# Optimization experiments

Hardware: AMD Instinct MI355X
Metric: run time of the kernel (lower is better)

The kernel has to match this reference:

```python
import jax, jax.numpy as jnp
import numpy as np

B, S, D = 4, 2048, 1024  # batch, seq_len, input_dim (= dk = dv)


def setup_inputs() -> dict:
    key = jax.random.key(0)
    kx, kq, kk, kv = jax.random.split(key, 4)
    scale = 1.0 / np.sqrt(D)
    return {
        "x": jax.random.normal(kx, (B, S, D), dtype=jnp.float32),
        "Wq": jax.random.normal(kq, (D, D), dtype=jnp.float32) * scale,
        "Wk": jax.random.normal(kk, (D, D), dtype=jnp.float32) * scale,
        "Wv": jax.random.normal(kv, (D, D), dtype=jnp.float32) * scale,
    }


def reference(x, Wq, Wk, Wv):
    # Linear projections (bias=False). W is [in, out].
    Q = jnp.einsum("bsd,de->bse", x, Wq)
    K = jnp.einsum("bsd,de->bse", x, Wk)
    V = jnp.einsum("bsd,de->bse", x, Wv)
    dk = Q.shape[-1]
    # scores: [B, S, S]
    scores = jnp.einsum("bqe,bke->bqk", Q, K) / jnp.sqrt(jnp.float32(dk))
    # causal mask: upper triangle (j > i) masked to -inf
    S_len = x.shape[1]
    causal = jnp.triu(jnp.ones((S_len, S_len), dtype=bool), k=1)
    scores = jnp.where(causal[None, :, :], -jnp.inf, scores)
    attn = jax.nn.softmax(scores, axis=-1)
    # dropout p=0.0 (eval): identity
    return jnp.einsum("bqk,bke->bqe", attn, V)
```

## Files before the change

### kernel.cpp

```cpp
#include <hip/hip_runtime.h>

#define S_LEN 2048
#define DMODEL 1024
#define NBATCH 4

typedef unsigned short u16;
typedef __bf16 bf16x8 __attribute__((ext_vector_type(8)));
typedef float f32x4 __attribute__((ext_vector_type(4)));

typedef __attribute__((address_space(3))) unsigned lds_u32;
typedef const __attribute__((address_space(1))) unsigned glb_u32;

__device__ __forceinline__ u16 f2bf(float f) {
  union { float f; unsigned u; } v;
  v.f = f;
  unsigned r = v.u + 0x7fffu + ((v.u >> 16) & 1u);
  return (u16)(r >> 16);
}

__device__ __forceinline__ float bf2f(u16 h) {
  union { unsigned u; float f; } v;
  v.u = ((unsigned)h) << 16;
  return v.f;
}

__global__ void convert_x_kernel(const float* __restrict__ x, u16* __restrict__ xb, long n) {
  long i = ((long)blockIdx.x * blockDim.x + threadIdx.x) * 4;
  long stride = (long)gridDim.x * blockDim.x * 4;
  for (; i < n; i += stride) {
    float4 v = *reinterpret_cast<const float4*>(x + i);
    ushort4 o;
    o.x = f2bf(v.x); o.y = f2bf(v.y); o.z = f2bf(v.z); o.w = f2bf(v.w);
    *reinterpret_cast<ushort4*>(xb + i) = o;
  }
}

__global__ void transpose_w_kernel(const float* __restrict__ W, u16* __restrict__ Wt) {
  __shared__ float tile[32][33];
  int tx = threadIdx.x, ty = threadIdx.y;
  int k0 = blockIdx.x * 32, n0 = blockIdx.y * 32;
#pragma unroll
  for (int i = 0; i < 32; i += 8)
    tile[ty + i][tx] = W[(long)(k0 + ty + i) * DMODEL + n0 + tx];
  __syncthreads();
#pragma unroll
  for (int i = 0; i < 32; i += 8)
    Wt[(long)(n0 + ty + i) * DMODEL + k0 + tx] = f2bf(tile[tx][ty + i]);
}


#define STG(SRCP, LD, ISB, H, T, BUFB) do { \
    const u16* _s = (SRCP) + (long)(H) * 128 * (LD) + (T) * 64; \
    char* _d = lds + (BUFB) * 65536 + ((ISB) ? 32768 : 0) + ((H) * 8 + w) * 2048; \
    __builtin_amdgcn_global_load_lds((glb_u32*)_s, (lds_u32*)_d, 16, 0, 0); \
    __builtin_amdgcn_global_load_lds((glb_u32*)(_s + 32), (lds_u32*)(_d + 1024), 16, 0, 0); \
  } while (0)

#define READ_A(QM) do { \
    _Pragma("unroll") \
    for (int _i = 0; _i < 4; ++_i) { \
      int _mp = (QM) * 8 + wm * 4 + _i; \
      af[_i][0] = *(const bf16x8*)(_Al + (_mp * 2 + 0) * 1024 + frag_off); \
      af[_i][1] = *(const bf16x8*)(_Al + (_mp * 2 + 1) * 1024 + frag_off); \
    } \
  } while (0)

#define READ_BQ(DST, QN) do { \
    _Pragma("unroll") \
    for (int _j = 0; _j < 2; ++_j) { \
      int _np = (QN) * 8 + wn * 2 + _j; \
      DST[_j][0] = *(const bf16x8*)(_Bl + (_np * 2 + 0) * 1024 + frag_off); \
      DST[_j][1] = *(const bf16x8*)(_Bl + (_np * 2 + 1) * 1024 + frag_off); \
    } \
  } while (0)

#define MFMA16(QM, QN, BREG) do { \
    _Pragma("unroll") \
    for (int _i = 0; _i < 4; ++_i) \
      _Pragma("unroll") \
      for (int _j = 0; _j < 2; ++_j) { \
        acc[QM][QN][_i][_j] = __builtin_amdgcn_mfma_f32_16x16x32_bf16(af[_i][0], BREG[_j][0], acc[QM][QN][_i][_j], 0, 0, 0); \
        acc[QM][QN][_i][_j] = __builtin_amdgcn_mfma_f32_16x16x32_bf16(af[_i][1], BREG[_j][1], acc[QM][QN][_i][_j], 0, 0, 0); \
      } \
  } while (0)

template<int CMODE, int CAUSAL>
__global__ __launch_bounds__(512, 2) void gemm256(
    const u16* __restrict__ A, const u16* __restrict__ B, void* __restrict__ Cptr,
    int lda, int ldb, int ldc, int Kdim,
    long sAz, long sBz, long sCz)
{
  int bm = blockIdx.x, bn = blockIdx.y, bz = blockIdx.z;
  if (CAUSAL == 1 && bn > bm) return;
  int Keff = Kdim;
  if (CAUSAL == 2) { int lim = (bm + 1) * 256; if (lim < Keff) Keff = lim; }
  int NT = Keff >> 6;

  const u16* Ab = A + (long)bz * sAz + (long)bm * 256 * lda;
  const u16* Bb = B + (long)bz * sBz + (long)bn * 256 * ldb;

  __shared__ char lds[131072];

  int tid = threadIdx.x;
  int lane = tid & 63, w = tid >> 6;
  int wm = w >> 2, wn = w & 3;
  int l15 = lane & 15, lhi = lane >> 4;
  int frag_off = (l15 * 64 + lhi * 16) ^ (((lane >> 3) & 1) << 5);

  int le = lane ^ ((lane >> 5) << 1);
  int lr = le >> 2;
  int kb = (le & 3) * 8;

  const u16* Asrc = Ab + (long)(w * 16 + lr) * lda + kb;
  const u16* Bsrc = Bb + (long)(w * 16 + lr) * ldb + kb;

  f32x4 acc[2][2][4][2];
#pragma unroll
  for (int a = 0; a < 2; ++a)
#pragma unroll
    for (int b = 0; b < 2; ++b)
#pragma unroll
      for (int c = 0; c < 4; ++c)
#pragma unroll
        for (int d = 0; d < 2; ++d)
          acc[a][b][c][d] = (f32x4){0.f, 0.f, 0.f, 0.f};

  STG(Asrc, lda, 0, 0, 0, 0); STG(Bsrc, ldb, 1, 0, 0, 0);
  STG(Asrc, lda, 0, 1, 0, 0); STG(Bsrc, ldb, 1, 1, 0, 0);
  STG(Asrc, lda, 0, 0, 1, 1); STG(Bsrc, ldb, 1, 0, 1, 1);
  asm volatile("s_waitcnt vmcnt(4)" ::: "memory");
  __builtin_amdgcn_s_barrier();

  for (int g = 0; g < NT; ++g) {
    int buf = g & 1;
    int t1 = g + 1; if (t1 >= NT) t1 -= NT;
    int t2 = g + 2; if (t2 >= NT) t2 -= NT;
    const char* _Al = lds + buf * 65536;
    const char* _Bl = _Al + 32768;
    bf16x8 af[4][2], b0[2][2], b1[2][2];

    READ_A(0);
    READ_BQ(b0, 0);
    STG(Asrc, lda, 0, 1, t1, buf ^ 1);
    __builtin_amdgcn_s_barrier();
    asm volatile("s_waitcnt lgkmcnt(0)" ::: "memory");
    __builtin_amdgcn_sched_barrier(0);
    __builtin_amdgcn_s_setprio(1);
    MFMA16(0, 0, b0);
    __builtin_amdgcn_s_setprio(0);
    __builtin_amdgcn_s_barrier();

    READ_BQ(b1, 1);
    STG(Bsrc, ldb, 1, 1, t1, buf ^ 1);
    __builtin_amdgcn_s_barrier();
    asm volatile("s_waitcnt lgkmcnt(0)" ::: "memory");
    __builtin_amdgcn_sched_barrier(0);
    __builtin_amdgcn_s_setprio(1);
    MFMA16(0, 1, b1);
    __builtin_amdgcn_s_setprio(0);
    __builtin_amdgcn_s_barrier();

    READ_A(1);
    STG(Asrc, lda, 0, 0, t2, buf);
    __builtin_amdgcn_s_barrier();
    asm volatile("s_waitcnt lgkmcnt(0)" ::: "memory");
    __builtin_amdgcn_sched_barrier(0);
    __builtin_amdgcn_s_setprio(1);
    MFMA16(1, 1, b1);
    __builtin_amdgcn_s_setprio(0);
    __builtin_amdgcn_s_barrier();

    STG(Bsrc, ldb, 1, 0, t2, buf);
    __builtin_amdgcn_s_barrier();
    __builtin_amdgcn_s_setprio(1);
    MFMA16(1, 0, b0);
    __builtin_amdgcn_s_setprio(0);
    asm volatile("s_waitcnt vmcnt(4)" ::: "memory");
    __builtin_amdgcn_s_barrier();
  }

  int Mbase = bm * 256, Nbase = bn * 256;
#pragma unroll
  for (int qm = 0; qm < 2; ++qm)
#pragma unroll
    for (int qn = 0; qn < 2; ++qn)
#pragma unroll
      for (int i = 0; i < 4; ++i)
#pragma unroll
        for (int j = 0; j < 2; ++j) {
          int r0 = Mbase + qm * 128 + wm * 64 + i * 16 + lhi * 4;
          int col = Nbase + qn * 128 + wn * 32 + j * 16 + l15;
          f32x4 v = acc[qm][qn][i][j];
          if constexpr (CMODE == 0) {
            float* C = (float*)Cptr + (long)bz * sCz;
#pragma unroll
            for (int r = 0; r < 4; ++r)
              C[(long)(r0 + r) * ldc + col] = v[r];
          } else if constexpr (CMODE == 1) {
            u16* C = (u16*)Cptr + (long)bz * sCz;
#pragma unroll
            for (int r = 0; r < 4; ++r)
              C[(long)(r0 + r) * ldc + col] = f2bf(v[r]);
          } else {
            if (col < 2048) {
              u16* dst = (u16*)Cptr + (col >= 1024 ? 8388608 : 0);
              int c = col & 1023;
#pragma unroll
              for (int r = 0; r < 4; ++r)
                dst[(long)(r0 + r) * 1024 + c] = f2bf(v[r]);
            } else {
              u16* Vt = (u16*)Cptr + 16777216;
              int e = col - 2048;
              int bb = r0 >> 11, s = r0 & 2047;
              ushort4 u;
              u.x = f2bf(v[0]); u.y = f2bf(v[1]); u.z = f2bf(v[2]); u.w = f2bf(v[3]);
              *reinterpret_cast<ushort4*>(Vt + ((long)bb * 1024 + e) * 2048 + s) = u;
            }
          }
        }
}

__global__ __launch_bounds__(256) void softmax1p(const u16* __restrict__ sc,
                                                 u16* __restrict__ P) {
  int q = blockIdx.x, b = blockIdx.y;
  const u16* srow = sc + ((long)b * S_LEN + q) * S_LEN;
  u16* prow = P + ((long)b * S_LEN + q) * S_LEN;
  int n = q + 1;
  int nz = ((q >> 8) + 1) << 8;
  int tid = threadIdx.x;
  int j0 = tid * 8;
  const float scale = 0.03125f;

  __shared__ float red[8];

  float vs[8];
#pragma unroll
  for (int e = 0; e < 8; ++e) vs[e] = -1e30f;
  if (j0 < n) {
    ushort4 a = *reinterpret_cast<const ushort4*>(srow + j0);
    ushort4 c = *reinterpret_cast<const ushort4*>(srow + j0 + 4);
    vs[0] = bf2f(a.x) * scale; vs[1] = bf2f(a.y) * scale;
    vs[2] = bf2f(a.z) * scale; vs[3] = bf2f(a.w) * scale;
    vs[4] = bf2f(c.x) * scale; vs[5] = bf2f(c.y) * scale;
    vs[6] = bf2f(c.z) * scale; vs[7] = bf2f(c.w) * scale;
#pragma unroll
    for (int e = 0; e < 8; ++e)
      if (j0 + e >= n) vs[e] = -1e30f;
  }

  float m = -1e30f;
#pragma unroll
  for (int e = 0; e < 8; ++e) m = fmaxf(m, vs[e]);
#pragma unroll
  for (int off = 32; off > 0; off >>= 1) m = fmaxf(m, __shfl_xor(m, off, 64));
  if ((tid & 63) == 0) red[tid >> 6] = m;
  __syncthreads();
  float ms = fmaxf(fmaxf(red[0], red[1]), fmaxf(red[2], red[3]));

  float p[8];
  float s = 0.f;
#pragma unroll
  for (int e = 0; e < 8; ++e) { p[e] = __expf(vs[e] - ms); s += (j0 + e < n) ? p[e] : 0.f; }
#pragma unroll
  for (int off = 32; off > 0; off >>= 1) s += __shfl_xor(s, off, 64);
  __syncthreads();
  if ((tid & 63) == 0) red[4 + (tid >> 6)] = s;
  __syncthreads();
  float inv = 1.f / (red[4] + red[5] + red[6] + red[7]);

  if (j0 < nz) {
    ushort4 o0, o1;
    o0.x = (j0 + 0 < n) ? f2bf(p[0] * inv) : (u16)0;
    o0.y = (j0 + 1 < n) ? f2bf(p[1] * inv) : (u16)0;
    o0.z = (j0 + 2 < n) ? f2bf(p[2] * inv) : (u16)0;
    o0.w = (j0 + 3 < n) ? f2bf(p[3] * inv) : (u16)0;
    o1.x = (j0 + 4 < n) ? f2bf(p[4] * inv) : (u16)0;
    o1.y = (j0 + 5 < n) ? f2bf(p[5] * inv) : (u16)0;
    o1.z = (j0 + 6 < n) ? f2bf(p[6] * inv) : (u16)0;
    o1.w = (j0 + 7 < n) ? f2bf(p[7] * inv) : (u16)0;
    *reinterpret_cast<ushort4*>(prow + j0) = o0;
    *reinterpret_cast<ushort4*>(prow + j0 + 4) = o1;
  }
}

extern "C" void kernel_launch(void* const* d_in, const int* in_sizes, int n_in,
                              void* d_out, int out_size, void* d_ws, size_t ws_size,
                              hipStream_t stream) {
  const float* x  = (const float*)d_in[0];
  const float* Wq = (const float*)d_in[1];
  const float* Wk = (const float*)d_in[2];
  const float* Wv = (const float*)d_in[3];
  float* out = (float*)d_out;

  char* ws = (char*)d_ws;
  u16* xb  = (u16*)(ws);
  u16* wtb = (u16*)(ws + 16777216);
  u16* Qb  = (u16*)(ws + 23068672);
  u16* Kb  = (u16*)(ws + 39845888);
  u16* Vtb = (u16*)(ws + 56623104);
  u16* scb = (u16*)(ws + 73400320);
  u16* P   = (u16*)(ws + 106954752);

  long nx = (long)NBATCH * S_LEN * DMODEL;
  convert_x_kernel<<<2048, 256, 0, stream>>>(x, xb, nx);

  dim3 tb(32, 8);
  transpose_w_kernel<<<dim3(32, 32), tb, 0, stream>>>(Wq, wtb);
  transpose_w_kernel<<<dim3(32, 32), tb, 0, stream>>>(Wk, wtb + 1024 * 1024);
  transpose_w_kernel<<<dim3(32, 32), tb, 0, stream>>>(Wv, wtb + 2 * 1024 * 1024);

  gemm256<3, 0><<<dim3(32, 12, 1), 512, 0, stream>>>(
      xb, wtb, Qb, DMODEL, DMODEL, 0, DMODEL, 0, 0, 0);

  gemm256<1, 1><<<dim3(8, 8, 4), 512, 0, stream>>>(
      Qb, Kb, scb, DMODEL, DMODEL, S_LEN, DMODEL,
      (long)S_LEN * DMODEL, (long)S_LEN * DMODEL, (long)S_LEN * S_LEN);

  softmax1p<<<dim3(S_LEN, NBATCH), 256, 0, stream>>>(scb, P);

  gemm256<0, 2><<<dim3(8, 4, 4), 512, 0, stream>>>(
      P, Vtb, out, S_LEN, S_LEN, DMODEL, S_LEN,
      (long)S_LEN * S_LEN, (long)DMODEL * S_LEN, (long)S_LEN * DMODEL);
}
```

Before: 185.7 us.

## Add XCD swizzle, 128-row BK32 GEMM, split-K causal PV, fused weight transpose

Adds an XCD-aware block remap to the GEMMs. The QKV projection and PV GEMMs move to a new 128x256 tile kernel with K-step 32 and triple buffering, so more blocks launch and load balance improves. The causal PV product is split into two K halves, with a separate add kernel summing the second-half partials into the output. The three weight-transpose launches are merged into one, and the softmax zero-fill granularity shrinks to 128 to match the new tiles. The trade-off is extra partial-sum traffic and one more launch.

```diff
diff --git a/kernel.cpp b/kernel.cpp
--- a/kernel.cpp
+++ b/kernel.cpp
@@ -23,6 +23,15 @@
   v.u = ((unsigned)h) << 16;
   return v.f;
 }
+
+#define XCD_SWZ() do { \
+    int _nwg = gridDim.x * gridDim.y * gridDim.z; \
+    int _hw = blockIdx.x + gridDim.x * (blockIdx.y + gridDim.y * blockIdx.z); \
+    int _q = _nwg >> 3; \
+    int _w = (_hw & 7) * _q + (_hw >> 3); \
+    bm = _w % gridDim.x; _w /= gridDim.x; \
+    bn = _w % gridDim.y; bz = _w / gridDim.y; \
+  } while (0)
 
 __global__ void convert_x_kernel(const float* __restrict__ x, u16* __restrict__ xb, long n) {
   long i = ((long)blockIdx.x * blockDim.x + threadIdx.x) * 4;
@@ -35,7 +44,10 @@
   }
 }
 
-__global__ void transpose_w_kernel(const float* __restrict__ W, u16* __restrict__ Wt) {
+__global__ void transpose_w3_kernel(const float* __restrict__ Wq, const float* __restrict__ Wk,
+                                    const float* __restrict__ Wv, u16* __restrict__ Wt) {
+  const float* W = blockIdx.z == 0 ? Wq : (blockIdx.z == 1 ? Wk : Wv);
+  u16* dst = Wt + (long)blockIdx.z * 1024 * 1024;
   __shared__ float tile[32][33];
   int tx = threadIdx.x, ty = threadIdx.y;
   int k0 = blockIdx.x * 32, n0 = blockIdx.y * 32;
@@ -45,9 +57,8 @@
   __syncthreads();
 #pragma unroll
   for (int i = 0; i < 32; i += 8)
-    Wt[(long)(n0 + ty + i) * DMODEL + k0 + tx] = f2bf(tile[tx][ty + i]);
-}
-
+    dst[(long)(n0 + ty + i) * DMODEL + k0 + tx] = f2bf(tile[tx][ty + i]);
+}
 
 #define STG(SRCP, LD, ISB, H, T, BUFB) do { \
     const u16* _s = (SRCP) + (long)(H) * 128 * (LD) + (T) * 64; \
@@ -84,17 +95,15 @@
       } \
   } while (0)
 
-template<int CMODE, int CAUSAL>
-__global__ __launch_bounds__(512, 2) void gemm256(
-    const u16* __restrict__ A, const u16* __restrict__ B, void* __restrict__ Cptr,
+__global__ __launch_bounds__(512, 2) void gemm256_sc(
+    const u16* __restrict__ A, const u16* __restrict__ B, u16* __restrict__ Cptr,
     int lda, int ldb, int ldc, int Kdim,
     long sAz, long sBz, long sCz)
 {
-  int bm = blockIdx.x, bn = blockIdx.y, bz = blockIdx.z;
-  if (CAUSAL == 1 && bn > bm) return;
-  int Keff = Kdim;
-  if (CAUSAL == 2) { int lim = (bm + 1) * 256; if (lim < Keff) Keff = lim; }
-  int NT = Keff >> 6;
+  int bm, bn, bz;
+  XCD_SWZ();
+  if (bn > bm) return;
+  int NT = Kdim >> 6;
 
   const u16* Ab = A + (long)bz * sAz + (long)bm * 256 * lda;
   const u16* Bb = B + (long)bz * sBz + (long)bn * 256 * ldb;
@@ -180,6 +189,7 @@
   }
 
   int Mbase = bm * 256, Nbase = bn * 256;
+  u16* C = Cptr + (long)bz * sCz;
 #pragma unroll
   for (int qm = 0; qm < 2; ++qm)
 #pragma unroll
@@ -191,33 +201,149 @@
           int r0 = Mbase + qm * 128 + wm * 64 + i * 16 + lhi * 4;
           int col = Nbase + qn * 128 + wn * 32 + j * 16 + l15;
           f32x4 v = acc[qm][qn][i][j];
-          if constexpr (CMODE == 0) {
-            float* C = (float*)Cptr + (long)bz * sCz;
-#pragma unroll
-            for (int r = 0; r < 4; ++r)
-              C[(long)(r0 + r) * ldc + col] = v[r];
-          } else if constexpr (CMODE == 1) {
-            u16* C = (u16*)Cptr + (long)bz * sCz;
-#pragma unroll
-            for (int r = 0; r < 4; ++r)
-              C[(long)(r0 + r) * ldc + col] = f2bf(v[r]);
-          } else {
-            if (col < 2048) {
-              u16* dst = (u16*)Cptr + (col >= 1024 ? 8388608 : 0);
-              int c = col & 1023;
-#pragma unroll
-              for (int r = 0; r < 4; ++r)
-                dst[(long)(r0 + r) * 1024 + c] = f2bf(v[r]);
-            } else {
-              u16* Vt = (u16*)Cptr + 16777216;
-              int e = col - 2048;
-              int bb = r0 >> 11, s = r0 & 2047;
-              ushort4 u;
-              u.x = f2bf(v[0]); u.y = f2bf(v[1]); u.z = f2bf(v[2]); u.w = f2bf(v[3]);
-              *reinterpret_cast<ushort4*>(Vt + ((long)bb * 1024 + e) * 2048 + s) = u;
-            }
-          }
+#pragma unroll
+          for (int r = 0; r < 4; ++r)
+            C[(long)(r0 + r) * ldc + col] = f2bf(v[r]);
         }
+}
+
+template<int CMODE, int MODE>
+__global__ __launch_bounds__(512) void gemm_bk32(
+    const u16* __restrict__ A, const u16* __restrict__ B,
+    void* __restrict__ Cptr, void* __restrict__ Cptr2,
+    int lda, int ldb, int ldc, int Kdim,
+    long sAz, long sBz, long sCz)
+{
+  int bm, bn, bz;
+  XCD_SWZ();
+  int k0 = 0, Keff = Kdim, h = 0;
+  if constexpr (MODE == 4) {
+    h = bz & 1;
+    bz >>= 1;
+    int Klim = (bm + 1) * 128;
+    k0 = h * 1024;
+    if (k0 >= Klim) return;
+    int k1 = k0 + 1024; if (k1 > Klim) k1 = Klim;
+    Keff = k1 - k0;
+  }
+  int NT = Keff >> 5;
+
+  const u16* Ab = A + (long)bz * sAz + (long)bm * 128 * lda + k0;
+  const u16* Bb = B + (long)bz * sBz + (long)bn * 256 * ldb + k0;
+
+  __shared__ char lds[73728];
+
+  int tid = threadIdx.x;
+  int lane = tid & 63, w = tid >> 6;
+  int wm = w >> 2, wn = w & 3;
+  int l15 = lane & 15, lhi = lane >> 4;
+  int frag_off = (l15 * 64 + lhi * 16) ^ (((lane >> 3) & 1) << 5);
+
+  int le = lane ^ ((lane >> 5) << 1);
+  int lr = le >> 2;
+  int kb = (le & 3) * 8;
+
+  const u16* Asrc = Ab + (long)(w * 16 + lr) * lda + kb;
+  const u16* Bsrc = Bb + (long)(w * 16 + lr) * ldb + kb;
+
+#define STG32(T, BI) do { \
+    const u16* _sa = Asrc + (T) * 32; \
+    const u16* _sb = Bsrc + (T) * 32; \
+    char* _base = lds + (BI) * 24576; \
+    __builtin_amdgcn_global_load_lds((glb_u32*)_sa, (lds_u32*)(_base + w * 1024), 16, 0, 0); \
+    __builtin_amdgcn_global_load_lds((glb_u32*)_sb, (lds_u32*)(_base + 8192 + w * 1024), 16, 0, 0); \
+    __builtin_amdgcn_global_load_lds((glb_u32*)(_sb + (long)128 * ldb), (lds_u32*)(_base + 8192 + (8 + w) * 1024), 16, 0, 0); \
+  } while (0)
+
+  f32x4 acc[4][4];
+#pragma unroll
+  for (int i = 0; i < 4; ++i)
+#pragma unroll
+    for (int j = 0; j < 4; ++j)
+      acc[i][j] = (f32x4){0.f, 0.f, 0.f, 0.f};
+
+  STG32(0, 0);
+  STG32(1, 1);
+  asm volatile("s_waitcnt vmcnt(3)" ::: "memory");
+  __builtin_amdgcn_s_barrier();
+
+  int buf = 0;
+  for (int g = 0; g < NT; ++g) {
+    bool issue = (g + 2 < NT);
+    if (issue) {
+      int b2 = buf + 2; if (b2 >= 3) b2 -= 3;
+      STG32(g + 2, b2);
+    }
+
+    const char* _Al = lds + buf * 24576;
+    const char* _Bl = _Al + 8192;
+    bf16x8 af[4], bf[4];
+#pragma unroll
+    for (int i = 0; i < 4; ++i)
+      af[i] = *(const bf16x8*)(_Al + (wm * 4 + i) * 1024 + frag_off);
+#pragma unroll
+    for (int j = 0; j < 4; ++j)
+      bf[j] = *(const bf16x8*)(_Bl + (wn * 4 + j) * 1024 + frag_off);
+
+    asm volatile("s_waitcnt lgkmcnt(0)" ::: "memory");
+    __builtin_amdgcn_sched_barrier(0);
+    __builtin_amdgcn_s_setprio(1);
+#pragma unroll
+    for (int i = 0; i < 4; ++i)
+#pragma unroll
+      for (int j = 0; j < 4; ++j)
+        acc[i][j] = __builtin_amdgcn_mfma_f32_16x16x32_bf16(af[i], bf[j], acc[i][j], 0, 0, 0);
+    __builtin_amdgcn_s_setprio(0);
+
+    if (issue) {
+      asm volatile("s_waitcnt vmcnt(3)" ::: "memory");
+    } else {
+      asm volatile("s_waitcnt vmcnt(0)" ::: "memory");
+    }
+    __builtin_amdgcn_s_barrier();
+
+    ++buf; if (buf >= 3) buf = 0;
+  }
+#undef STG32
+
+#pragma unroll
+  for (int i = 0; i < 4; ++i)
+#pragma unroll
+    for (int j = 0; j < 4; ++j) {
+      int rl = wm * 64 + i * 16 + lhi * 4;
+      int col = bn * 256 + wn * 64 + j * 16 + l15;
+      f32x4 v = acc[i][j];
+      if constexpr (CMODE == 5) {
+        if (h == 0) {
+          float* O = (float*)Cptr2 + (long)bz * S_LEN * 1024;
+          int row = bm * 128 + rl;
+#pragma unroll
+          for (int r = 0; r < 4; ++r)
+            O[(long)(row + r) * 1024 + col] = v[r];
+        } else {
+          float* Pp = (float*)Cptr + ((long)((bz * 8 + bm - 8) * 128 + rl)) * 1024 + col;
+#pragma unroll
+          for (int r = 0; r < 4; ++r)
+            Pp[(long)r * 1024] = v[r];
+        }
+      } else {
+        int r0 = bm * 128 + rl;
+        if (col < 2048) {
+          u16* dst = (u16*)Cptr + (col >= 1024 ? 8388608 : 0);
+          int c = col & 1023;
+#pragma unroll
+          for (int r = 0; r < 4; ++r)
+            dst[(long)(r0 + r) * 1024 + c] = f2bf(v[r]);
+        } else {
+          u16* Vt = (u16*)Cptr + 16777216;
+          int e = col - 2048;
+          int bb = r0 >> 11, s = r0 & 2047;
+          ushort4 u;
+          u.x = f2bf(v[0]); u.y = f2bf(v[1]); u.z = f2bf(v[2]); u.w = f2bf(v[3]);
+          *reinterpret_cast<ushort4*>(Vt + ((long)bb * 1024 + e) * 2048 + s) = u;
+        }
+      }
+    }
 }
 
 __global__ __launch_bounds__(256) void softmax1p(const u16* __restrict__ sc,
@@ -226,7 +352,7 @@
   const u16* srow = sc + ((long)b * S_LEN + q) * S_LEN;
   u16* prow = P + ((long)b * S_LEN + q) * S_LEN;
   int n = q + 1;
-  int nz = ((q >> 8) + 1) << 8;
+  int nz = ((q >> 7) + 1) << 7;
   int tid = threadIdx.x;
   int j0 = tid * 8;
   const float scale = 0.03125f;
@@ -283,6 +409,18 @@
   }
 }
 
+__global__ __launch_bounds__(256) void add_pv(const float4* __restrict__ p2,
+                                              float4* __restrict__ out) {
+  long i = (long)blockIdx.x * 256 + threadIdx.x;
+  int c4 = (int)(i & 255);
+  long rp = i >> 8;
+  int b = (int)(rp >> 10), r = (int)(rp & 1023);
+  long oo = ((long)(b * 2048 + 1024 + r) << 8) + c4;
+  float4 a = out[oo], d = p2[i];
+  a.x += d.x; a.y += d.y; a.z += d.z; a.w += d.w;
+  out[oo] = a;
+}
+
 extern "C" void kernel_launch(void* const* d_in, const int* in_sizes, int n_in,
                               void* d_out, int out_size, void* d_ws, size_t ws_size,
                               hipStream_t stream) {
@@ -293,32 +431,32 @@
   float* out = (float*)d_out;
 
   char* ws = (char*)d_ws;
-  u16* xb  = (u16*)(ws);
-  u16* wtb = (u16*)(ws + 16777216);
-  u16* Qb  = (u16*)(ws + 23068672);
-  u16* Kb  = (u16*)(ws + 39845888);
-  u16* Vtb = (u16*)(ws + 56623104);
-  u16* scb = (u16*)(ws + 73400320);
-  u16* P   = (u16*)(ws + 106954752);
+  u16*   xb    = (u16*)(ws);
+  u16*   wtb   = (u16*)(ws + 16777216);
+  u16*   Qb    = (u16*)(ws + 23068672);
+  u16*   Kb    = (u16*)(ws + 39845888);
+  u16*   Vtb   = (u16*)(ws + 56623104);
+  u16*   scb   = (u16*)(ws + 73400320);
+  float* part2 = (float*)(ws + 73400320);
+  u16*   P     = (u16*)(ws + 115343360);
 
   long nx = (long)NBATCH * S_LEN * DMODEL;
   convert_x_kernel<<<2048, 256, 0, stream>>>(x, xb, nx);
 
-  dim3 tb(32, 8);
-  transpose_w_kernel<<<dim3(32, 32), tb, 0, stream>>>(Wq, wtb);
-  transpose_w_kernel<<<dim3(32, 32), tb, 0, stream>>>(Wk, wtb + 1024 * 1024);
-  transpose_w_kernel<<<dim3(32, 32), tb, 0, stream>>>(Wv, wtb + 2 * 1024 * 1024);
-
-  gemm256<3, 0><<<dim3(32, 12, 1), 512, 0, stream>>>(
-      xb, wtb, Qb, DMODEL, DMODEL, 0, DMODEL, 0, 0, 0);
-
-  gemm256<1, 1><<<dim3(8, 8, 4), 512, 0, stream>>>(
+  transpose_w3_kernel<<<dim3(32, 32, 3), dim3(32, 8), 0, stream>>>(Wq, Wk, Wv, wtb);
+
+  gemm_bk32<3, 0><<<dim3(64, 12, 1), 512, 0, stream>>>(
+      xb, wtb, Qb, nullptr, DMODEL, DMODEL, 0, DMODEL, 0, 0, 0);
+
+  gemm256_sc<<<dim3(8, 8, 4), 512, 0, stream>>>(
       Qb, Kb, scb, DMODEL, DMODEL, S_LEN, DMODEL,
       (long)S_LEN * DMODEL, (long)S_LEN * DMODEL, (long)S_LEN * S_LEN);
 
   softmax1p<<<dim3(S_LEN, NBATCH), 256, 0, stream>>>(scb, P);
 
-  gemm256<0, 2><<<dim3(8, 4, 4), 512, 0, stream>>>(
-      P, Vtb, out, S_LEN, S_LEN, DMODEL, S_LEN,
-      (long)S_LEN * S_LEN, (long)DMODEL * S_LEN, (long)S_LEN * DMODEL);
-}
+  gemm_bk32<5, 4><<<dim3(16, 4, 8), 512, 0, stream>>>(
+      P, Vtb, part2, out, S_LEN, S_LEN, 0, S_LEN,
+      (long)S_LEN * S_LEN, (long)DMODEL * S_LEN, 0);
+
+  add_pv<<<4096, 256, 0, stream>>>((const float4*)part2, (float4*)out);
+}
```

Result: faster. 173.7 us (-6.5%).
